# Kernel optimization log

Hardware: AMD Instinct MI355X
Metric: run time of the kernel (lower is better)

## Reference

```python
import jax, jax.numpy as jnp
import numpy as np
import math

NUM_HEADS = 8
EPS = 1e-12  # torch F.normalize eps


def _l2norm(x):
    # torch F.normalize(x, dim=-1): x / max(||x||_2, eps)
    n = jnp.sqrt(jnp.sum(x * x, axis=-1, keepdims=True))
    return x / jnp.maximum(n, EPS)


def setup_inputs() -> dict:
    key = jax.random.key(0)
    ks = jax.random.split(key, 8)
    b, t, l, c = 8, 256, 24, 512
    s = 1.0 / math.sqrt(c)
    return {
        "q": jax.random.normal(ks[0], (b, t, l, c), jnp.float32),
        "kv": jax.random.normal(ks[1], (b, t, l, c), jnp.float32),
        "Wq": jax.random.normal(ks[2], (c, c), jnp.float32) * s,
        "bq": jnp.zeros((c,), jnp.float32),
        "Wkv": jax.random.normal(ks[3], (c, 2 * c), jnp.float32) * s,
        "bkv": jnp.zeros((2 * c,), jnp.float32),
        "Wg": jax.random.normal(ks[4], (c, c), jnp.float32) * s,
        "bg": jnp.zeros((c,), jnp.float32),
        "v_init": _l2norm(jax.random.normal(ks[5], (1, 1, l, c), jnp.float32) * s),
        "Wm": jax.random.normal(ks[6], (c, c), jnp.float32) * s,
        "bm": jnp.zeros((c,), jnp.float32),
    }


def reference(q, kv, Wq, bq, Wkv, bkv, Wg, bg, v_init, Wm, bm):
    b, t, l, c = q.shape
    H = NUM_HEADS
    d = c // H
    shortcut = q

    # q projection -> heads -> cosine normalize
    qh = (q @ Wq + bq).reshape(b, t, l, H, d).transpose(0, 1, 3, 2, 4)  # [b,t,H,l,d]
    qh = _l2norm(qh)

    # k, v_lin from kv projection
    kvp = kv @ Wkv + bkv                   # [b,t,l,2c]
    k_lin, v_lin = jnp.split(kvp, 2, axis=-1)
    kh = k_lin.reshape(b, t, l, H, d).transpose(0, 1, 3, 2, 4)
    kh = _l2norm(kh)

    # gated/tanh-modulated v: relu(sigmoid(Wg v_lin) * tanh(v_init))
    gate = jax.nn.sigmoid(v_lin @ Wg + bg)  # [b,t,l,c]
    vp = jnp.broadcast_to(v_init, (b, t, l, c))
    v = jax.nn.relu(gate * jnp.tanh(vp)).reshape(b, t, l, H, d).transpose(0, 1, 3, 2, 4)
    v = _l2norm(v)

    # attention (dropout in eval mode -> identity)
    atten = jnp.einsum('bthqd,bthkd->bthqk', qh, kh) / math.sqrt(d)
    atten = jax.nn.softmax(atten, axis=-1)
    x = jnp.einsum('bthqk,bthkd->bthqd', atten, v)   # [b,t,H,l,d]

    x = x.transpose(0, 1, 3, 2, 4).reshape(b, t, l, c)
    return (x @ Wm + bm) + shortcut
```

## Files before the change

kernel.cpp:

```cpp
#include <hip/hip_runtime.h>
#include <math.h>

typedef unsigned short u16;
typedef __attribute__((ext_vector_type(8))) short s16x8;
typedef __attribute__((ext_vector_type(4))) float f32x4;

#define NB 8
#define NT 256
#define NL 24
#define NC 512
#define NH 8
#define ND 64
#define NR (NB*NT*NL)
#define NBT (NB*NT)

__device__ __forceinline__ u16 f2bf(float f) {
    unsigned u = __float_as_uint(f);
    u = (u + 0x7fffu + ((u >> 16) & 1u)) >> 16;
    return (u16)u;
}
__device__ __forceinline__ float bf2f(u16 h) {
    return __uint_as_float(((unsigned)h) << 16);
}

__global__ void convert_kernel(const float* __restrict__ q, const float* __restrict__ kv,
                               const float* __restrict__ Wq, const float* __restrict__ Wkv,
                               const float* __restrict__ Wg, const float* __restrict__ Wm,
                               const float* __restrict__ v_init,
                               u16* __restrict__ qbf, u16* __restrict__ kvbf,
                               u16* __restrict__ Wq_t, u16* __restrict__ Wkv_t,
                               u16* __restrict__ Wg_t, u16* __restrict__ Wm_t,
                               float* __restrict__ tvi)
{
    const int stride = gridDim.x * blockDim.x;
    const int t0 = blockIdx.x * blockDim.x + threadIdx.x;

    const long long n4 = (long long)NR * NC / 4;
    for (long long i = t0; i < n4; i += stride) {
        float4 a = ((const float4*)q)[i];
        ushort4 oa;
        oa.x = f2bf(a.x); oa.y = f2bf(a.y); oa.z = f2bf(a.z); oa.w = f2bf(a.w);
        ((ushort4*)qbf)[i] = oa;
        float4 b = ((const float4*)kv)[i];
        ushort4 ob;
        ob.x = f2bf(b.x); ob.y = f2bf(b.y); ob.z = f2bf(b.z); ob.w = f2bf(b.w);
        ((ushort4*)kvbf)[i] = ob;
    }
    for (int e = t0; e < 512 * 512; e += stride) {
        int n = e >> 9, k = e & 511;
        Wq_t[e] = f2bf(Wq[k * 512 + n]);
        Wg_t[e] = f2bf(Wg[k * 512 + n]);
        Wm_t[e] = f2bf(Wm[k * 512 + n]);
    }
    for (int e = t0; e < 1024 * 512; e += stride) {
        int n = e >> 9, k = e & 511;
        Wkv_t[e] = f2bf(Wkv[k * 1024 + n]);
    }
    for (int e = t0; e < NL * NC; e += stride) {
        tvi[e] = tanhf(v_init[e]);
    }
}

template <int MODE>
__global__ __launch_bounds__(256)
void gemm_kernel(const u16* __restrict__ A, int lda,
                 const u16* __restrict__ Bt,
                 const float* __restrict__ bias,
                 void* __restrict__ out, int ldo,
                 const float* __restrict__ extra)
{
    __shared__ __align__(16) u16 Alds[3][128 * 32];
    __shared__ __align__(16) u16 Blds[3][128 * 32];

    const int tid = threadIdx.x;
    const int mb = blockIdx.x, nb = blockIdx.y;
    const int wave = tid >> 6, lane = tid & 63;
    const int wr = wave >> 1, wc = wave & 1;
    const int lrow = lane & 15;
    const int lg = lane >> 4;
    const int rko = (lg ^ ((lrow >> 1) & 3)) * 8;

    f32x4 acc[4][4] = {};

    const int row_a[2] = { tid >> 2, (256 + tid) >> 2 };
    const int k8s = (((tid & 3) ^ ((tid >> 3) & 3)) * 8);

#define STAGE(buf, k0)                                                          \
    do {                                                                        \
        _Pragma("unroll")                                                       \
        for (int c = 0; c < 2; ++c) {                                           \
            const u16* srcA = A + (size_t)(mb * 128 + row_a[c]) * lda + (k0) + k8s; \
            u16* dstA = &Alds[buf][(c * 256 + wave * 64) * 8];                  \
            __builtin_amdgcn_global_load_lds(                                   \
                (const __attribute__((address_space(1))) void*)srcA,            \
                (__attribute__((address_space(3))) void*)dstA, 16, 0, 0);       \
        }                                                                       \
        _Pragma("unroll")                                                       \
        for (int c = 0; c < 2; ++c) {                                           \
            const u16* srcB = Bt + (size_t)(nb * 128 + row_a[c]) * 512 + (k0) + k8s; \
            u16* dstB = &Blds[buf][(c * 256 + wave * 64) * 8];                  \
            __builtin_amdgcn_global_load_lds(                                   \
                (const __attribute__((address_space(1))) void*)srcB,            \
                (__attribute__((address_space(3))) void*)dstB, 16, 0, 0);       \
        }                                                                       \
    } while (0)

    STAGE(0, 0);
    STAGE(1, 32);

#pragma unroll
    for (int t = 0; t < 16; ++t) {
        if (t < 15) asm volatile("s_waitcnt vmcnt(4)" ::: "memory");
        else        asm volatile("s_waitcnt vmcnt(0)" ::: "memory");
        __builtin_amdgcn_s_barrier();

        const int cb = t % 3;
        s16x8 af[4], bfr[4];
#pragma unroll
        for (int m = 0; m < 4; ++m)
            af[m] = *(const s16x8*)&Alds[cb][(wr * 64 + m * 16 + lrow) * 32 + rko];
#pragma unroll
        for (int n = 0; n < 4; ++n)
            bfr[n] = *(const s16x8*)&Blds[cb][(wc * 64 + n * 16 + lrow) * 32 + rko];
#pragma unroll
        for (int m = 0; m < 4; ++m)
#pragma unroll
            for (int n = 0; n < 4; ++n)
                acc[m][n] = __builtin_amdgcn_mfma_f32_16x16x32_bf16(
                    bfr[n], af[m], acc[m][n], 0, 0, 0);

        if (t < 14) STAGE((t + 2) % 3, (t + 2) * 32);
    }
#undef STAGE

    const int rbase = mb * 128 + wr * 64;
    const int cbase = nb * 128 + wc * 64;
#pragma unroll
    for (int m = 0; m < 4; ++m) {
        const int row = rbase + m * 16 + lrow;
#pragma unroll
        for (int n = 0; n < 4; ++n) {
            const int col0 = cbase + n * 16 + lg * 4;
            float4 bv = *(const float4*)&bias[col0];
            float v0 = acc[m][n][0] + bv.x;
            float v1 = acc[m][n][1] + bv.y;
            float v2 = acc[m][n][2] + bv.z;
            float v3 = acc[m][n][3] + bv.w;
            if constexpr (MODE == 0 || MODE == 1) {
                ushort4 o = { f2bf(v0), f2bf(v1), f2bf(v2), f2bf(v3) };
                *(ushort4*)&((u16*)out)[(size_t)row * ldo + col0] = o;
            } else if constexpr (MODE == 2) {
                float4 tv = *(const float4*)&extra[(row % NL) * NC + col0];
                float g0 = 1.f / (1.f + __expf(-v0));
                float g1 = 1.f / (1.f + __expf(-v1));
                float g2 = 1.f / (1.f + __expf(-v2));
                float g3 = 1.f / (1.f + __expf(-v3));
                ushort4 o = { f2bf(fmaxf(g0 * tv.x, 0.f)), f2bf(fmaxf(g1 * tv.y, 0.f)),
                              f2bf(fmaxf(g2 * tv.z, 0.f)), f2bf(fmaxf(g3 * tv.w, 0.f)) };
                *(ushort4*)&((u16*)out)[(size_t)row * ldo + col0] = o;
            } else {
                float4 sc = *(const float4*)&extra[(size_t)row * NC + col0];
                float4 o = { v0 + sc.x, v1 + sc.y, v2 + sc.z, v3 + sc.w };
                *(float4*)&((float*)out)[(size_t)row * ldo + col0] = o;
            }
        }
    }
}

__global__ __launch_bounds__(256)
void attn_kernel(const u16* __restrict__ qp, const u16* __restrict__ kvp,
                 const u16* __restrict__ vun, u16* __restrict__ xout)
{
    __shared__ __align__(16) u16 Plds[4][32 * 32];
    __shared__ __align__(16) u16 VTlds[4][64 * 32];

    const int tid = threadIdx.x;
    const int wave = tid >> 6, lane = tid & 63;
    const int lr = lane & 15, lg = lane >> 4;
    const size_t rowbase = (size_t)blockIdx.x * NL;
    u16* P  = Plds[wave];
    u16* VT = VTlds[wave];

    for (int hh = 0; hh < 2; ++hh) {
        const int h = wave * 2 + hh;

        s16x8 qf[2][2], kf[2][2], vf[2][2];
#pragma unroll
        for (int m = 0; m < 2; ++m) {
            int rq = m * 16 + lr; int r = rq > 23 ? 23 : rq;
            const u16* q_ = qp  + (rowbase + r) * 512  + h * 64 + lg * 8;
            const u16* k_ = kvp + (rowbase + r) * 1024 + h * 64 + lg * 8;
            const u16* v_ = vun + (rowbase + r) * 512  + h * 64 + lg * 8;
#pragma unroll
            for (int ks = 0; ks < 2; ++ks) {
                qf[m][ks] = *(const s16x8*)(q_ + ks * 32);
                kf[m][ks] = *(const s16x8*)(k_ + ks * 32);
                vf[m][ks] = *(const s16x8*)(v_ + ks * 32);
            }
        }

        float invq[2], invk[2], invv[2];
#pragma unroll
        for (int m = 0; m < 2; ++m) {
            float sq = 0.f, sk = 0.f, sv = 0.f;
#pragma unroll
            for (int ks = 0; ks < 2; ++ks)
#pragma unroll
                for (int j = 0; j < 8; ++j) {
                    float a = bf2f((u16)qf[m][ks][j]); sq += a * a;
                    float b = bf2f((u16)kf[m][ks][j]); sk += b * b;
                    float c = bf2f((u16)vf[m][ks][j]); sv += c * c;
                }
            sq += __shfl_xor(sq, 16); sq += __shfl_xor(sq, 32);
            sk += __shfl_xor(sk, 16); sk += __shfl_xor(sk, 32);
            sv += __shfl_xor(sv, 16); sv += __shfl_xor(sv, 32);
            invq[m] = 1.f / fmaxf(sqrtf(sq), 1e-12f);
            invk[m] = 1.f / fmaxf(sqrtf(sk), 1e-12f);
            invv[m] = 1.f / fmaxf(sqrtf(sv), 1e-12f);
        }

        f32x4 sc[2][2] = {};
#pragma unroll
        for (int m = 0; m < 2; ++m)
#pragma unroll
            for (int n = 0; n < 2; ++n)
#pragma unroll
                for (int ks = 0; ks < 2; ++ks)
                    sc[m][n] = __builtin_amdgcn_mfma_f32_16x16x32_bf16(
                        qf[m][ks], kf[n][ks], sc[m][n], 0, 0, 0);

#pragma unroll
        for (int m = 0; m < 2; ++m) {
#pragma unroll
            for (int j = 0; j < 4; ++j) {
                float nq = __shfl(invq[m], lg * 4 + j);
                float a0 = sc[m][0][j] * nq * invk[0] * 0.125f;
                float a1 = (lr < 8) ? sc[m][1][j] * nq * invk[1] * 0.125f : -3.0e38f;
                float mx = fmaxf(a0, a1);
#pragma unroll
                for (int d = 1; d < 16; d <<= 1) mx = fmaxf(mx, __shfl_xor(mx, d));
                float e0 = __expf(a0 - mx);
                float e1 = (lr < 8) ? __expf(a1 - mx) : 0.f;
                float s = e0 + e1;
#pragma unroll
                for (int d = 1; d < 16; d <<= 1) s += __shfl_xor(s, d);
                float inv = 1.f / s;
                int r = m * 16 + lg * 4 + j;
                P[r * 32 + lr]      = f2bf(e0 * inv);
                P[r * 32 + 16 + lr] = f2bf(e1 * inv);
            }
        }

#pragma unroll
        for (int m = 0; m < 2; ++m)
#pragma unroll
            for (int ks = 0; ks < 2; ++ks)
#pragma unroll
                for (int j = 0; j < 8; ++j) {
                    int c = ks * 32 + lg * 8 + j;
                    int r = m * 16 + lr;
                    VT[c * 32 + r] = f2bf(bf2f((u16)vf[m][ks][j]) * invv[m]);
                }

        asm volatile("s_waitcnt lgkmcnt(0)" ::: "memory");
        __builtin_amdgcn_sched_barrier(0);

        s16x8 pa[2], vb[4];
#pragma unroll
        for (int m = 0; m < 2; ++m)
            pa[m] = *(const s16x8*)&P[(m * 16 + lr) * 32 + lg * 8];
#pragma unroll
        for (int n = 0; n < 4; ++n)
            vb[n] = *(const s16x8*)&VT[(n * 16 + lr) * 32 + lg * 8];

        f32x4 xa[2][4] = {};
#pragma unroll
        for (int m = 0; m < 2; ++m)
#pragma unroll
            for (int n = 0; n < 4; ++n)
                xa[m][n] = __builtin_amdgcn_mfma_f32_16x16x32_bf16(
                    pa[m], vb[n], xa[m][n], 0, 0, 0);

#pragma unroll
        for (int m = 0; m < 2; ++m)
#pragma unroll
            for (int n = 0; n < 4; ++n)
#pragma unroll
                for (int j = 0; j < 4; ++j) {
                    int r = m * 16 + lg * 4 + j;
                    if (r < 24)
                        xout[(rowbase + r) * 512 + h * 64 + n * 16 + lr] =
                            f2bf(xa[m][n][j]);
                }

        asm volatile("s_waitcnt lgkmcnt(0)" ::: "memory");
        __builtin_amdgcn_sched_barrier(0);
    }
}

extern "C" void kernel_launch(void* const* d_in, const int* in_sizes, int n_in,
                              void* d_out, int out_size, void* d_ws, size_t ws_size,
                              hipStream_t stream)
{
    const float* q      = (const float*)d_in[0];
    const float* kv     = (const float*)d_in[1];
    const float* Wq     = (const float*)d_in[2];
    const float* bq     = (const float*)d_in[3];
    const float* Wkv    = (const float*)d_in[4];
    const float* bkv    = (const float*)d_in[5];
    const float* Wg     = (const float*)d_in[6];
    const float* bg     = (const float*)d_in[7];
    const float* v_init = (const float*)d_in[8];
    const float* Wm     = (const float*)d_in[9];
    const float* bm     = (const float*)d_in[10];

    char* ws = (char*)d_ws;
    const size_t SZ = (size_t)NR * NC;
    u16* buf0   = (u16*)(ws);
    u16* buf1   = (u16*)(ws + 2 * SZ);
    u16* qp     = (u16*)(ws + 4 * SZ);
    u16* kvp    = (u16*)(ws + 6 * SZ);
    char* wbase = ws + 10 * SZ;
    u16* Wq_t   = (u16*)(wbase);
    u16* Wkv_t  = (u16*)(wbase + 512 * 512 * 2);
    u16* Wg_t   = (u16*)(wbase + 512 * 512 * 2 + 1024 * 512 * 2);
    u16* Wm_t   = (u16*)(wbase + 2 * 512 * 512 * 2 + 1024 * 512 * 2);
    float* tvi  = (float*)(wbase + 3 * 512 * 512 * 2 + 1024 * 512 * 2);

    convert_kernel<<<1024, 256, 0, stream>>>(q, kv, Wq, Wkv, Wg, Wm, v_init,
                                             buf0, buf1, Wq_t, Wkv_t, Wg_t, Wm_t, tvi);

    gemm_kernel<1><<<dim3(NR / 128, 8), 256, 0, stream>>>(buf1, 512, Wkv_t, bkv,
                                                          kvp, 1024, nullptr);
    gemm_kernel<0><<<dim3(NR / 128, 4), 256, 0, stream>>>(buf0, 512, Wq_t, bq,
                                                          qp, 512, nullptr);
    gemm_kernel<2><<<dim3(NR / 128, 4), 256, 0, stream>>>(kvp + 512, 1024, Wg_t, bg,
                                                          buf1, 512, tvi);

    attn_kernel<<<dim3(NBT), 256, 0, stream>>>(qp, kvp, buf1, buf0);

    gemm_kernel<3><<<dim3(NR / 128, 4), 256, 0, stream>>>(buf0, 512, Wm_t, bm,
                                                          d_out, 512, q);
}
```

Baseline: 580.7 us.

## Add 512-thread double-buffered GEMM and XCD-aware block swizzle for projections

Introduces a new 512-thread GEMM variant with 8 waves per 128x128 tile, each wave computing 64x32, using double-buffered LDS staging with explicit barriers. The first three projection GEMMs switch to it, and all GEMMs now use a 1D grid remapped so consecutive blocks spread across the 8 XCDs while neighbouring tiles share A rows for L2 reuse. The epilogue is factored into a shared helper. The aim is more waves per CU and better cache locality, at the cost of fewer accumulators per wave and an extra barrier per k-step.

```diff
diff --git a/kernel.cpp b/kernel.cpp
--- a/kernel.cpp
+++ b/kernel.cpp
@@ -13,6 +13,7 @@
 #define ND 64
 #define NR (NB*NT*NL)
 #define NBT (NB*NT)
+#define NMB (NR/128)
 
 __device__ __forceinline__ u16 f2bf(float f) {
     unsigned u = __float_as_uint(f);
@@ -62,18 +63,132 @@
 }
 
 template <int MODE>
+__device__ __forceinline__ void epilogue_store(
+    const f32x4& a, int row, int col0, const float* bias,
+    void* out, int ldo, const float* extra)
+{
+    float4 bv = *(const float4*)&bias[col0];
+    float v0 = a[0] + bv.x, v1 = a[1] + bv.y, v2 = a[2] + bv.z, v3 = a[3] + bv.w;
+    if constexpr (MODE == 0 || MODE == 1) {
+        ushort4 o = { f2bf(v0), f2bf(v1), f2bf(v2), f2bf(v3) };
+        *(ushort4*)&((u16*)out)[(size_t)row * ldo + col0] = o;
+    } else if constexpr (MODE == 2) {
+        float4 tv = *(const float4*)&extra[(row % NL) * NC + col0];
+        float g0 = 1.f / (1.f + __expf(-v0));
+        float g1 = 1.f / (1.f + __expf(-v1));
+        float g2 = 1.f / (1.f + __expf(-v2));
+        float g3 = 1.f / (1.f + __expf(-v3));
+        ushort4 o = { f2bf(fmaxf(g0 * tv.x, 0.f)), f2bf(fmaxf(g1 * tv.y, 0.f)),
+                      f2bf(fmaxf(g2 * tv.z, 0.f)), f2bf(fmaxf(g3 * tv.w, 0.f)) };
+        *(ushort4*)&((u16*)out)[(size_t)row * ldo + col0] = o;
+    } else {
+        float4 sc = *(const float4*)&extra[(size_t)row * NC + col0];
+        float4 o = { v0 + sc.x, v1 + sc.y, v2 + sc.z, v3 + sc.w };
+        *(float4*)&((float*)out)[(size_t)row * ldo + col0] = o;
+    }
+}
+
+template <int MODE, int NNB_LOG2>
+__global__ __launch_bounds__(512)
+void gemm_db(const u16* __restrict__ A, int lda,
+             const u16* __restrict__ Bt,
+             const float* __restrict__ bias,
+             void* __restrict__ out, int ldo,
+             const float* __restrict__ extra)
+{
+    __shared__ __align__(16) u16 Alds[2][128 * 32];
+    __shared__ __align__(16) u16 Blds[2][128 * 32];
+
+    const int tid = threadIdx.x;
+    const int cpx = (NMB << NNB_LOG2) >> 3;
+    const int wgl = blockIdx.x;
+    const int swz = (wgl & 7) * cpx + (wgl >> 3);
+    const int nb = swz & ((1 << NNB_LOG2) - 1);
+    const int mb = swz >> NNB_LOG2;
+
+    const int wave = tid >> 6, lane = tid & 63;
+    const int wr = wave >> 2, wc = wave & 3;
+    const int lrow = lane & 15, lg = lane >> 4;
+    const int rko = (lg ^ ((lrow >> 1) & 3)) * 8;
+
+    f32x4 acc[4][2] = {};
+
+    const int srow = tid >> 2;
+    const int k8s = (((tid & 3) ^ ((tid >> 3) & 3)) * 8);
+
+#define STAGE(buf, k0)                                                          \
+    do {                                                                        \
+        const u16* srcA = A + (size_t)(mb * 128 + srow) * lda + (k0) + k8s;     \
+        u16* dstA = &Alds[buf][wave * 64 * 8];           \
+        __builtin_amdgcn_global_load_lds(                                       \
+            (const __attribute__((address_space(1))) void*)srcA,                \
+            (__attribute__((address_space(3))) void*)dstA, 16, 0, 0);           \
+        const u16* srcB = Bt + (size_t)(nb * 128 + srow) * 512 + (k0) + k8s;    \
+        u16* dstB = &Blds[buf][wave * 64 * 8];                                  \
+        __builtin_amdgcn_global_load_lds(                                       \
+            (const __attribute__((address_space(1))) void*)srcB,                \
+            (__attribute__((address_space(3))) void*)dstB, 16, 0, 0);           \
+    } while (0)
+
+    STAGE(0, 0);
+    STAGE(1, 32);
+
+#pragma unroll
+    for (int t = 0; t < 16; ++t) {
+        if (t < 15) asm volatile("s_waitcnt vmcnt(2)" ::: "memory");
+        else        asm volatile("s_waitcnt vmcnt(0)" ::: "memory");
+        __builtin_amdgcn_s_barrier();
+
+        const int cb = t & 1;
+        s16x8 bfr[2];
+#pragma unroll
+        for (int n = 0; n < 2; ++n)
+            bfr[n] = *(const s16x8*)&Blds[cb][(wc * 32 + n * 16 + lrow) * 32 + rko];
+#pragma unroll
+        for (int m = 0; m < 4; ++m) {
+            s16x8 af = *(const s16x8*)&Alds[cb][(wr * 64 + m * 16 + lrow) * 32 + rko];
+#pragma unroll
+            for (int n = 0; n < 2; ++n)
+                acc[m][n] = __builtin_amdgcn_mfma_f32_16x16x32_bf16(
+                    bfr[n], af, acc[m][n], 0, 0, 0);
+        }
+
+        asm volatile("s_waitcnt lgkmcnt(0)" ::: "memory");
+        __builtin_amdgcn_s_barrier();
+        if (t < 14) STAGE(t & 1, (t + 2) * 32);
+    }
+#undef STAGE
+
+    const int rbase = mb * 128 + wr * 64;
+    const int cbase = nb * 128 + wc * 32;
+#pragma unroll
+    for (int m = 0; m < 4; ++m) {
+        const int row = rbase + m * 16 + lrow;
+#pragma unroll
+        for (int n = 0; n < 2; ++n)
+            epilogue_store<MODE>(acc[m][n], row, cbase + n * 16 + lg * 4,
+                                 bias, out, ldo, extra);
+    }
+}
+
+template <int MODE, int NNB_LOG2>
 __global__ __launch_bounds__(256)
-void gemm_kernel(const u16* __restrict__ A, int lda,
-                 const u16* __restrict__ Bt,
-                 const float* __restrict__ bias,
-                 void* __restrict__ out, int ldo,
-                 const float* __restrict__ extra)
+void gemm_tb(const u16* __restrict__ A, int lda,
+             const u16* __restrict__ Bt,
+             const float* __restrict__ bias,
+             void* __restrict__ out, int ldo,
+             const float* __restrict__ extra)
 {
     __shared__ __align__(16) u16 Alds[3][128 * 32];
     __shared__ __align__(16) u16 Blds[3][128 * 32];
 
     const int tid = threadIdx.x;
-    const int mb = blockIdx.x, nb = blockIdx.y;
+    const int cpx = (NMB << NNB_LOG2) >> 3;
+    const int wgl = blockIdx.x;
+    const int swz = (wgl & 7) * cpx + (wgl >> 3);
+    const int nb = swz & ((1 << NNB_LOG2) - 1);
+    const int mb = swz >> NNB_LOG2;
+
     const int wave = tid >> 6, lane = tid & 63;
     const int wr = wave >> 1, wc = wave & 1;
     const int lrow = lane & 15;
@@ -139,31 +254,9 @@
     for (int m = 0; m < 4; ++m) {
         const int row = rbase + m * 16 + lrow;
 #pragma unroll
-        for (int n = 0; n < 4; ++n) {
-            const int col0 = cbase + n * 16 + lg * 4;
-            float4 bv = *(const float4*)&bias[col0];
-            float v0 = acc[m][n][0] + bv.x;
-            float v1 = acc[m][n][1] + bv.y;
-            float v2 = acc[m][n][2] + bv.z;
-            float v3 = acc[m][n][3] + bv.w;
-            if constexpr (MODE == 0 || MODE == 1) {
-                ushort4 o = { f2bf(v0), f2bf(v1), f2bf(v2), f2bf(v3) };
-                *(ushort4*)&((u16*)out)[(size_t)row * ldo + col0] = o;
-            } else if constexpr (MODE == 2) {
-                float4 tv = *(const float4*)&extra[(row % NL) * NC + col0];
-                float g0 = 1.f / (1.f + __expf(-v0));
-                float g1 = 1.f / (1.f + __expf(-v1));
-                float g2 = 1.f / (1.f + __expf(-v2));
-                float g3 = 1.f / (1.f + __expf(-v3));
-                ushort4 o = { f2bf(fmaxf(g0 * tv.x, 0.f)), f2bf(fmaxf(g1 * tv.y, 0.f)),
-                              f2bf(fmaxf(g2 * tv.z, 0.f)), f2bf(fmaxf(g3 * tv.w, 0.f)) };
-                *(ushort4*)&((u16*)out)[(size_t)row * ldo + col0] = o;
-            } else {
-                float4 sc = *(const float4*)&extra[(size_t)row * NC + col0];
-                float4 o = { v0 + sc.x, v1 + sc.y, v2 + sc.z, v3 + sc.w };
-                *(float4*)&((float*)out)[(size_t)row * ldo + col0] = o;
-            }
-        }
+        for (int n = 0; n < 4; ++n)
+            epilogue_store<MODE>(acc[m][n], row, cbase + n * 16 + lg * 4,
+                                 bias, out, ldo, extra);
     }
 }
 
@@ -330,15 +423,15 @@
     convert_kernel<<<1024, 256, 0, stream>>>(q, kv, Wq, Wkv, Wg, Wm, v_init,
                                              buf0, buf1, Wq_t, Wkv_t, Wg_t, Wm_t, tvi);
 
-    gemm_kernel<1><<<dim3(NR / 128, 8), 256, 0, stream>>>(buf1, 512, Wkv_t, bkv,
-                                                          kvp, 1024, nullptr);
-    gemm_kernel<0><<<dim3(NR / 128, 4), 256, 0, stream>>>(buf0, 512, Wq_t, bq,
-                                                          qp, 512, nullptr);
-    gemm_kernel<2><<<dim3(NR / 128, 4), 256, 0, stream>>>(kvp + 512, 1024, Wg_t, bg,
-                                                          buf1, 512, tvi);
+    gemm_db<1, 3><<<NMB * 8, 512, 0, stream>>>(buf1, 512, Wkv_t, bkv,
+                                               kvp, 1024, nullptr);
+    gemm_db<0, 2><<<NMB * 4, 512, 0, stream>>>(buf0, 512, Wq_t, bq,
+                                               qp, 512, nullptr);
+    gemm_db<2, 2><<<NMB * 4, 512, 0, stream>>>(kvp + 512, 1024, Wg_t, bg,
+                                               buf1, 512, tvi);
 
     attn_kernel<<<dim3(NBT), 256, 0, stream>>>(qp, kvp, buf1, buf0);
 
-    gemm_kernel<3><<<dim3(NR / 128, 4), 256, 0, stream>>>(buf0, 512, Wm_t, bm,
-                                                          d_out, 512, q);
-}
+    gemm_tb<3, 2><<<NMB * 4, 256, 0, stream>>>(buf0, 512, Wm_t, bm,
+                                               d_out, 512, q);
+}
```

Result: no change. 578.2 us (-0.4%).

## Use 128x256 GEMM tiles with 512 threads, double buffering and XCD-aware block swizzle

Applied to the files above, without the earlier changes.

Replaces the 128x128 triple-buffered GEMM with a 512-thread kernel computing 128x256 tiles using two LDS buffers and an extra barrier before refilling. Block indices are remapped so consecutive blocks land on the same XCD. The larger N tile halves the number of A-tile re-reads, and the swizzle aims to improve L2 locality. The cost is an extra barrier per k-step and shallower prefetch depth.

```diff
diff --git a/kernel.cpp b/kernel.cpp
--- a/kernel.cpp
+++ b/kernel.cpp
@@ -13,6 +13,7 @@
 #define ND 64
 #define NR (NB*NT*NL)
 #define NBT (NB*NT)
+#define NMB (NR/128)
 
 __device__ __forceinline__ u16 f2bf(float f) {
     unsigned u = __float_as_uint(f);
@@ -62,43 +63,70 @@
 }
 
 template <int MODE>
-__global__ __launch_bounds__(256)
-void gemm_kernel(const u16* __restrict__ A, int lda,
-                 const u16* __restrict__ Bt,
-                 const float* __restrict__ bias,
-                 void* __restrict__ out, int ldo,
-                 const float* __restrict__ extra)
-{
-    __shared__ __align__(16) u16 Alds[3][128 * 32];
-    __shared__ __align__(16) u16 Blds[3][128 * 32];
+__device__ __forceinline__ void epilogue_store(
+    const f32x4& a, int row, int col0, const float* bias,
+    void* out, int ldo, const float* extra)
+{
+    float4 bv = *(const float4*)&bias[col0];
+    float v0 = a[0] + bv.x, v1 = a[1] + bv.y, v2 = a[2] + bv.z, v3 = a[3] + bv.w;
+    if constexpr (MODE == 0 || MODE == 1) {
+        ushort4 o = { f2bf(v0), f2bf(v1), f2bf(v2), f2bf(v3) };
+        *(ushort4*)&((u16*)out)[(size_t)row * ldo + col0] = o;
+    } else if constexpr (MODE == 2) {
+        float4 tv = *(const float4*)&extra[(row % NL) * NC + col0];
+        float g0 = 1.f / (1.f + __expf(-v0));
+        float g1 = 1.f / (1.f + __expf(-v1));
+        float g2 = 1.f / (1.f + __expf(-v2));
+        float g3 = 1.f / (1.f + __expf(-v3));
+        ushort4 o = { f2bf(fmaxf(g0 * tv.x, 0.f)), f2bf(fmaxf(g1 * tv.y, 0.f)),
+                      f2bf(fmaxf(g2 * tv.z, 0.f)), f2bf(fmaxf(g3 * tv.w, 0.f)) };
+        *(ushort4*)&((u16*)out)[(size_t)row * ldo + col0] = o;
+    } else {
+        float4 sc = *(const float4*)&extra[(size_t)row * NC + col0];
+        float4 o = { v0 + sc.x, v1 + sc.y, v2 + sc.z, v3 + sc.w };
+        *(float4*)&((float*)out)[(size_t)row * ldo + col0] = o;
+    }
+}
+
+template <int MODE, int NNB_LOG2>
+__global__ __launch_bounds__(512)
+void gemm_db(const u16* __restrict__ A, int lda,
+             const u16* __restrict__ Bt,
+             const float* __restrict__ bias,
+             void* __restrict__ out, int ldo,
+             const float* __restrict__ extra)
+{
+    __shared__ __align__(16) u16 Alds[2][128 * 32];
+    __shared__ __align__(16) u16 Blds[2][256 * 32];
 
     const int tid = threadIdx.x;
-    const int mb = blockIdx.x, nb = blockIdx.y;
+    const int cpx = (NMB << NNB_LOG2) >> 3;
+    const int wgl = blockIdx.x;
+    const int swz = (wgl & 7) * cpx + (wgl >> 3);
+    const int nb = swz & ((1 << NNB_LOG2) - 1);
+    const int mb = swz >> NNB_LOG2;
+
     const int wave = tid >> 6, lane = tid & 63;
-    const int wr = wave >> 1, wc = wave & 1;
-    const int lrow = lane & 15;
-    const int lg = lane >> 4;
+    const int wr = wave >> 2, wc = wave & 3;
+    const int lrow = lane & 15, lg = lane >> 4;
     const int rko = (lg ^ ((lrow >> 1) & 3)) * 8;
 
     f32x4 acc[4][4] = {};
 
-    const int row_a[2] = { tid >> 2, (256 + tid) >> 2 };
+    const int srow = tid >> 2;
     const int k8s = (((tid & 3) ^ ((tid >> 3) & 3)) * 8);
 
 #define STAGE(buf, k0)                                                          \
     do {                                                                        \
+        const u16* srcA = A + (size_t)(mb * 128 + srow) * lda + (k0) + k8s;     \
+        u16* dstA = &Alds[buf][wave * 64 * 8];           \
+        __builtin_amdgcn_global_load_lds(                                       \
+            (const __attribute__((address_space(1))) void*)srcA,                \
+            (__attribute__((address_space(3))) void*)dstA, 16, 0, 0);           \
         _Pragma("unroll")                                                       \
         for (int c = 0; c < 2; ++c) {                                           \
-            const u16* srcA = A + (size_t)(mb * 128 + row_a[c]) * lda + (k0) + k8s; \
-            u16* dstA = &Alds[buf][(c * 256 + wave * 64) * 8];                  \
-            __builtin_amdgcn_global_load_lds(                                   \
-                (const __attribute__((address_space(1))) void*)srcA,            \
-                (__attribute__((address_space(3))) void*)dstA, 16, 0, 0);       \
-        }                                                                       \
-        _Pragma("unroll")                                                       \
-        for (int c = 0; c < 2; ++c) {                                           \
-            const u16* srcB = Bt + (size_t)(nb * 128 + row_a[c]) * 512 + (k0) + k8s; \
-            u16* dstB = &Blds[buf][(c * 256 + wave * 64) * 8];                  \
+            const u16* srcB = Bt + (size_t)(nb * 256 + c * 128 + srow) * 512 + (k0) + k8s; \
+            u16* dstB = &Blds[buf][(c * 512 + wave * 64) * 8];                  \
             __builtin_amdgcn_global_load_lds(                                   \
                 (const __attribute__((address_space(1))) void*)srcB,            \
                 (__attribute__((address_space(3))) void*)dstB, 16, 0, 0);       \
@@ -110,11 +138,11 @@
 
 #pragma unroll
     for (int t = 0; t < 16; ++t) {
-        if (t < 15) asm volatile("s_waitcnt vmcnt(4)" ::: "memory");
+        if (t < 15) asm volatile("s_waitcnt vmcnt(3)" ::: "memory");
         else        asm volatile("s_waitcnt vmcnt(0)" ::: "memory");
         __builtin_amdgcn_s_barrier();
 
-        const int cb = t % 3;
+        const int cb = t & 1;
         s16x8 af[4], bfr[4];
 #pragma unroll
         for (int m = 0; m < 4; ++m)
@@ -129,41 +157,21 @@
                 acc[m][n] = __builtin_amdgcn_mfma_f32_16x16x32_bf16(
                     bfr[n], af[m], acc[m][n], 0, 0, 0);
 
-        if (t < 14) STAGE((t + 2) % 3, (t + 2) * 32);
+        asm volatile("s_waitcnt lgkmcnt(0)" ::: "memory");
+        __builtin_amdgcn_s_barrier();
+        if (t < 14) STAGE(t & 1, (t + 2) * 32);
     }
 #undef STAGE
 
     const int rbase = mb * 128 + wr * 64;
-    const int cbase = nb * 128 + wc * 64;
+    const int cbase = nb * 256 + wc * 64;
 #pragma unroll
     for (int m = 0; m < 4; ++m) {
         const int row = rbase + m * 16 + lrow;
 #pragma unroll
-        for (int n = 0; n < 4; ++n) {
-            const int col0 = cbase + n * 16 + lg * 4;
-            float4 bv = *(const float4*)&bias[col0];
-            float v0 = acc[m][n][0] + bv.x;
-            float v1 = acc[m][n][1] + bv.y;
-            float v2 = acc[m][n][2] + bv.z;
-            float v3 = acc[m][n][3] + bv.w;
-            if constexpr (MODE == 0 || MODE == 1) {
-                ushort4 o = { f2bf(v0), f2bf(v1), f2bf(v2), f2bf(v3) };
-                *(ushort4*)&((u16*)out)[(size_t)row * ldo + col0] = o;
-            } else if constexpr (MODE == 2) {
-                float4 tv = *(const float4*)&extra[(row % NL) * NC + col0];
-                float g0 = 1.f / (1.f + __expf(-v0));
-                float g1 = 1.f / (1.f + __expf(-v1));
-                float g2 = 1.f / (1.f + __expf(-v2));
-                float g3 = 1.f / (1.f + __expf(-v3));
-                ushort4 o = { f2bf(fmaxf(g0 * tv.x, 0.f)), f2bf(fmaxf(g1 * tv.y, 0.f)),
-                              f2bf(fmaxf(g2 * tv.z, 0.f)), f2bf(fmaxf(g3 * tv.w, 0.f)) };
-                *(ushort4*)&((u16*)out)[(size_t)row * ldo + col0] = o;
-            } else {
-                float4 sc = *(const float4*)&extra[(size_t)row * NC + col0];
-                float4 o = { v0 + sc.x, v1 + sc.y, v2 + sc.z, v3 + sc.w };
-                *(float4*)&((float*)out)[(size_t)row * ldo + col0] = o;
-            }
-        }
+        for (int n = 0; n < 4; ++n)
+            epilogue_store<MODE>(acc[m][n], row, cbase + n * 16 + lg * 4,
+                                 bias, out, ldo, extra);
     }
 }
 
@@ -330,15 +338,15 @@
     convert_kernel<<<1024, 256, 0, stream>>>(q, kv, Wq, Wkv, Wg, Wm, v_init,
                                              buf0, buf1, Wq_t, Wkv_t, Wg_t, Wm_t, tvi);
 
-    gemm_kernel<1><<<dim3(NR / 128, 8), 256, 0, stream>>>(buf1, 512, Wkv_t, bkv,
-                                                          kvp, 1024, nullptr);
-    gemm_kernel<0><<<dim3(NR / 128, 4), 256, 0, stream>>>(buf0, 512, Wq_t, bq,
-                                                          qp, 512, nullptr);
-    gemm_kernel<2><<<dim3(NR / 128, 4), 256, 0, stream>>>(kvp + 512, 1024, Wg_t, bg,
-                                                          buf1, 512, tvi);
+    gemm_db<1, 2><<<NMB * 4, 512, 0, stream>>>(buf1, 512, Wkv_t, bkv,
+                                               kvp, 1024, nullptr);
+    gemm_db<0, 1><<<NMB * 2, 512, 0, stream>>>(buf0, 512, Wq_t, bq,
+                                               qp, 512, nullptr);
+    gemm_db<2, 1><<<NMB * 2, 512, 0, stream>>>(kvp + 512, 1024, Wg_t, bg,
+                                               buf1, 512, tvi);
 
     attn_kernel<<<dim3(NBT), 256, 0, stream>>>(qp, kvp, buf1, buf0);
 
-    gemm_kernel<3><<<dim3(NR / 128, 4), 256, 0, stream>>>(buf0, 512, Wm_t, bm,
-                                                          d_out, 512, q);
-}
+    gemm_db<3, 1><<<NMB * 2, 512, 0, stream>>>(buf0, 512, Wm_t, bm,
+                                               d_out, 512, q);
+}
```

Result: slower. 611.0 us (+5.2%).
